# Performance work log

Hardware: AMD Instinct MI355X
Metric: run time of the kernel (lower is better)

## Reference

```python
import jax, jax.numpy as jnp
import numpy as np

D_IN, D_HIDDEN, DT_RANK, D_MEM, STEP = 256, 64, 16, 128, 16
B_, L_ = 2, 2048
S = 0.02  # weight init scale

def generate_a(d_in, d_hidden):
    i = jnp.arange(d_in, dtype=jnp.float32)[:, None]
    j = jnp.arange(d_hidden, dtype=jnp.float32)[None, :]
    off = jnp.sqrt(2.0 * i + 1.0) * jnp.sqrt(2.0 * j + 1.0)
    return jnp.where(i == j, i + 1.0, jnp.where(i > j, off, 0.0))

def setup_inputs():
    key = jax.random.key(0)
    ks = jax.random.split(key, 10)
    d_out = 3 * D_HIDDEN + 2 * D_IN + 2 * DT_RANK
    return {
        "x": jax.random.normal(ks[0], (B_, L_, D_IN), jnp.float32),
        "W_xproj": jax.random.normal(ks[1], (D_IN, d_out), jnp.float32) * S,
        "W_dt": jax.random.normal(ks[2], (DT_RANK, D_IN), jnp.float32) * S,
        "b_dt": jnp.full((D_IN,), -11.0, jnp.float32),
        "W_dtl": jax.random.normal(ks[3], (DT_RANK, D_IN), jnp.float32) * S,
        "b_dtl": jnp.full((D_IN,), -11.0, jnp.float32),
        "A": generate_a(D_IN, D_HIDDEN),
        "Dp": jnp.ones((D_IN,), jnp.float32),
        "W_Q": jax.random.normal(ks[4], (D_IN, D_MEM), jnp.float32) * S,
        "b_Q": jnp.zeros((D_MEM,), jnp.float32),
        "W_K": jax.random.normal(ks[5], (D_IN, D_MEM), jnp.float32) * S,
        "b_K": jnp.zeros((D_MEM,), jnp.float32),
        "W_V": jax.random.normal(ks[6], (D_IN, D_MEM), jnp.float32) * S,
        "b_V": jnp.zeros((D_MEM,), jnp.float32),
        "W_O": jax.random.normal(ks[7], (D_MEM, D_IN), jnp.float32) * S,
        "b_O": jnp.zeros((D_IN,), jnp.float32),
    }

def _selective_scan(u, delta, A, Bm, Cm, Dp):
    # u, delta: (b,l,d); A: (d,n); Bm, Cm: (b,l,n)
    dA = jnp.exp(jnp.einsum('bld,dn->bldn', delta, A))          # (b,l,d,n)
    dBu = delta[..., None] * Bm[:, :, None, :] * u[..., None]   # (b,l,d,n)
    def comb(e1, e2):
        a1, b1 = e1
        a2, b2 = e2
        return a2 * a1, a2 * b1 + b2
    _, xs = jax.lax.associative_scan(comb, (dA, dBu), axis=1)   # states (b,l,d,n)
    y = jnp.einsum('bldn,bln->bld', xs, Cm)
    if Dp is not None:
        y = y + u * Dp
    return y

def reference(x, W_xproj, W_dt, b_dt, W_dtl, b_dtl, A, Dp, W_Q, b_Q, W_K, b_K, W_V, b_V, W_O, b_O):
    proj = x @ W_xproj  # (b,l,3n+2d+2r)
    splits = np.cumsum([D_HIDDEN, D_HIDDEN, D_HIDDEN, D_IN, D_IN, DT_RANK]).tolist()
    Bm, Bl, Cm, E, Fg, dt, dtl = jnp.split(proj, splits, axis=-1)
    delta = jax.nn.softplus(dt @ W_dt + b_dt)       # delta_softplus=True folded in
    delta_l = jax.nn.softplus(dtl @ W_dtl + b_dtl)
    y = _selective_scan(x, delta, A, Bm, Cm, Dp)
    y_local = _selective_scan(x, delta_l, A, Bl, jnp.ones_like(Bl), None)  # C=ones, D=None
    memory = y_local[:, ::STEP, :]                  # strided checkpoints (b,m,d)
    Q = x @ W_Q + b_Q
    K = memory @ W_K + b_K
    V = memory @ W_V + b_V
    # note: original scales by sqrt(d_hidden), not sqrt(d_memory)
    w = jax.nn.softmax(jnp.einsum('blm,bkm->blk', Q, K) / jnp.sqrt(jnp.float32(D_HIDDEN)), axis=-1)
    att = jnp.einsum('blk,bkm->blm', w, V) @ W_O + b_O
    return y + att * E + x * Fg
```

## Files before the change

### kernel.cpp

```cpp
#include <hip/hip_runtime.h>
#include <math.h>

#define D_INN 256
#define D_HID 64
#define DTR 16
#define D_MEMM 128
#define BB 2
#define LL 2048
#define NROWS (BB*LL)
#define NPROJ 736
#define NTOT 864
#define SEG 16
#define SEGLEN (LL/SEG)

typedef __attribute__((ext_vector_type(8))) short short8v;
typedef __attribute__((ext_vector_type(4))) float float4v;

static __device__ __forceinline__ unsigned short f2bf(float f) {
    unsigned int u = __float_as_uint(f);
    u += 0x7fff + ((u >> 16) & 1);
    return (unsigned short)(u >> 16);
}

__global__ __launch_bounds__(256) void k_gemm(const float* __restrict__ x,
        const float* __restrict__ Wx, const float* __restrict__ Wq,
        const float* __restrict__ bq, float* __restrict__ proj) {
    __shared__ unsigned short As[64][40];
    __shared__ unsigned short Bs[64][40];
    const int t = threadIdx.x;
    const int lane = t & 63, w = t >> 6;
    const int wr = w >> 1, wc = w & 1;
    const int row0 = blockIdx.y * 64, col0 = blockIdx.x * 64;

    float4v acc[2][2];
    #pragma unroll
    for (int i = 0; i < 2; i++)
        #pragma unroll
        for (int j = 0; j < 2; j++) acc[i][j] = (float4v)0.f;

    const int ar = t >> 2, akq = (t & 3) * 8;
    const int bk = t >> 3, bcq = (t & 7) * 8;

    for (int k0 = 0; k0 < D_INN; k0 += 32) {
        float4 a0 = *(const float4*)&x[(size_t)(row0 + ar) * D_INN + k0 + akq];
        float4 a1 = *(const float4*)&x[(size_t)(row0 + ar) * D_INN + k0 + akq + 4];
        float4 b0 = {}, b1 = {};
        int col = col0 + bcq;
        if (col + 8 <= NPROJ) {
            b0 = *(const float4*)&Wx[(size_t)(k0 + bk) * NPROJ + col];
            b1 = *(const float4*)&Wx[(size_t)(k0 + bk) * NPROJ + col + 4];
        } else if (col < NTOT) {
            b0 = *(const float4*)&Wq[(size_t)(k0 + bk) * D_MEMM + (col - NPROJ)];
            b1 = *(const float4*)&Wq[(size_t)(k0 + bk) * D_MEMM + (col - NPROJ) + 4];
        }
        __syncthreads();
        {
            unsigned short av[8] = { f2bf(a0.x), f2bf(a0.y), f2bf(a0.z), f2bf(a0.w),
                                     f2bf(a1.x), f2bf(a1.y), f2bf(a1.z), f2bf(a1.w) };
            *(short8v*)&As[ar][akq] = *(short8v*)av;
            Bs[bcq + 0][bk] = f2bf(b0.x); Bs[bcq + 1][bk] = f2bf(b0.y);
            Bs[bcq + 2][bk] = f2bf(b0.z); Bs[bcq + 3][bk] = f2bf(b0.w);
            Bs[bcq + 4][bk] = f2bf(b1.x); Bs[bcq + 5][bk] = f2bf(b1.y);
            Bs[bcq + 6][bk] = f2bf(b1.z); Bs[bcq + 7][bk] = f2bf(b1.w);
        }
        __syncthreads();
        short8v af[2], bf[2];
        const int fr = lane & 15, fk = (lane >> 4) * 8;
        af[0] = *(short8v*)&As[wr * 32 + fr][fk];
        af[1] = *(short8v*)&As[wr * 32 + 16 + fr][fk];
        bf[0] = *(short8v*)&Bs[wc * 32 + fr][fk];
        bf[1] = *(short8v*)&Bs[wc * 32 + 16 + fr][fk];
        #pragma unroll
        for (int i = 0; i < 2; i++)
            #pragma unroll
            for (int j = 0; j < 2; j++)
                acc[i][j] = __builtin_amdgcn_mfma_f32_16x16x32_bf16(af[i], bf[j], acc[i][j], 0, 0, 0);
    }
    #pragma unroll
    for (int i = 0; i < 2; i++)
        #pragma unroll
        for (int j = 0; j < 2; j++)
            #pragma unroll
            for (int e = 0; e < 4; e++) {
                int rr = row0 + wr * 32 + i * 16 + (lane >> 4) * 4 + e;
                int cc = col0 + wc * 32 + j * 16 + (lane & 15);
                if (cc < NTOT) {
                    float v = acc[i][j][e];
                    if (cc >= NPROJ) v += bq[cc - NPROJ];
                    proj[(size_t)rr * NTOT + cc] = v;
                }
            }
}

__global__ __launch_bounds__(256) void k_delta(const float* __restrict__ proj,
        const float* __restrict__ Wdt, const float* __restrict__ bdt,
        const float* __restrict__ Wdtl, const float* __restrict__ bdtl,
        float* __restrict__ delta, float* __restrict__ deltal) {
    __shared__ float sdt[16][17], sdtl[16][17];
    const int t = threadIdx.x;
    const int r0 = blockIdx.x * 16;
    {
        int r = t >> 4, c = t & 15;
        sdt[r][c]  = proj[(size_t)(r0 + r) * NTOT + 704 + c];
        sdtl[r][c] = proj[(size_t)(r0 + r) * NTOT + 720 + c];
    }
    __syncthreads();
    float w1[DTR], w2[DTR];
    #pragma unroll
    for (int r = 0; r < DTR; r++) {
        w1[r] = Wdt[r * D_INN + t];
        w2[r] = Wdtl[r * D_INN + t];
    }
    const float b1 = bdt[t], b2 = bdtl[t];
    #pragma unroll
    for (int row = 0; row < 16; ++row) {
        float a1 = b1, a2 = b2;
        #pragma unroll
        for (int r = 0; r < DTR; r++) {
            a1 += sdt[row][r] * w1[r];
            a2 += sdtl[row][r] * w2[r];
        }
        delta[(size_t)(r0 + row) * D_INN + t]  = (a1 > 20.f) ? a1 : log1pf(expf(a1));
        deltal[(size_t)(r0 + row) * D_INN + t] = (a2 > 20.f) ? a2 : log1pf(expf(a2));
    }
}

__global__ __launch_bounds__(256) void k_scan1(const float* __restrict__ x,
        const float* __restrict__ proj, const float* __restrict__ A,
        const float* __restrict__ delta, const float* __restrict__ deltal,
        float* __restrict__ Qbuf, float* __restrict__ SDbuf,
        float* __restrict__ cumd, float* __restrict__ mem) {
    const int t = threadIdx.x;
    const int w = t >> 6, n = t & 63;
    const int b = blockIdx.y;
    const int scan = blockIdx.z >> 4, seg = blockIdx.z & 15;
    const int d = blockIdx.x * 4 + w;
    const size_t rowbase = (size_t)b * LL + (size_t)seg * SEGLEN;
    const float* dsel = (scan == 0 ? delta : deltal);
    const int cB = (scan == 0) ? 0 : 64;
    const float Aln = A[d * D_HID + n] * 1.44269504f;
    const int lr = n & 7;

    float s = 0.f, sd = 0.f;
    for (int c = 0; c < SEGLEN / 8; ++c) {
        const size_t l0 = rowbase + c * 8;
        float dvl = dsel[(l0 + lr) * D_INN + d];
        float pl  = dvl * x[(l0 + lr) * D_INN + d];
        float Bv[8];
        #pragma unroll
        for (int li = 0; li < 8; ++li) Bv[li] = proj[(l0 + li) * NTOT + cB + n];
        #pragma unroll
        for (int li = 0; li < 8; ++li) {
            float dv = __shfl(dvl, li);
            float p  = __shfl(pl, li);
            s = fmaf(exp2f(dv * Aln), s, p * Bv[li]);
            sd += dv;
            if (scan == 1 && li == 0 && (c & 1) == 0) {
                float v = s;
                #pragma unroll
                for (int off = 32; off >= 1; off >>= 1) v += __shfl_xor(v, off);
                if (n == 0) {
                    int k = seg * 8 + (c >> 1);
                    mem[((size_t)b * 128 + k) * D_INN + d] = v;
                    cumd[(((size_t)b * SEG + seg) * 8 + (c >> 1)) * D_INN + d] = sd;
                }
            }
        }
    }
    Qbuf[((((size_t)scan * 2 + b) * SEG + seg) * D_INN + d) * 64 + n] = s;
    if (n == 0) SDbuf[(((size_t)scan * 2 + b) * SEG + seg) * D_INN + d] = sd;
}

__global__ __launch_bounds__(256) void k_scan2(const float* __restrict__ x,
        const float* __restrict__ proj, const float* __restrict__ A,
        const float* __restrict__ Dp, const float* __restrict__ delta,
        const float* __restrict__ Qbuf, const float* __restrict__ SDbuf,
        float* __restrict__ y) {
    __shared__ float rbuf[4][8][65];
    const int t = threadIdx.x;
    const int w = t >> 6, n = t & 63;
    const int b = blockIdx.y, seg = blockIdx.z;
    const int d = blockIdx.x * 4 + w;
    const size_t rowbase = (size_t)b * LL + (size_t)seg * SEGLEN;
    const float Aln = A[d * D_HID + n] * 1.44269504f;
    const float Dpv = Dp[d];
    const int lr = n & 7;
    const int rli = n >> 3, g = n & 7;

    float s = 0.f;
    for (int k = 0; k < seg; ++k) {
        float sdk = SDbuf[(((size_t)b * SEG + k) * D_INN + d)];
        float Qk = Qbuf[(((size_t)b * SEG + k) * D_INN + d) * 64 + n];
        s = fmaf(exp2f(sdk * Aln), s, Qk);
    }

    for (int c = 0; c < SEGLEN / 8; ++c) {
        const size_t l0 = rowbase + c * 8;
        float dvl = delta[(l0 + lr) * D_INN + d];
        float uvl = x[(l0 + lr) * D_INN + d];
        float pl = dvl * uvl;
        float Bv[8], Cv[8];
        #pragma unroll
        for (int li = 0; li < 8; ++li) {
            Bv[li] = proj[(l0 + li) * NTOT + n];
            Cv[li] = proj[(l0 + li) * NTOT + 128 + n];
        }
        #pragma unroll
        for (int li = 0; li < 8; ++li) {
            float dv = __shfl(dvl, li);
            float p  = __shfl(pl, li);
            s = fmaf(exp2f(dv * Aln), s, p * Bv[li]);
            rbuf[w][li][n] = s * Cv[li];
        }
        float acc = 0.f;
        #pragma unroll
        for (int j = 0; j < 8; ++j) acc += rbuf[w][rli][g * 8 + j];
        acc += __shfl_xor(acc, 1);
        acc += __shfl_xor(acc, 2);
        acc += __shfl_xor(acc, 4);
        float uv = __shfl(uvl, rli);
        if (g == 0) {
            y[(l0 + rli) * D_INN + d] = acc + uv * Dpv;
        }
    }
}

__global__ __launch_bounds__(256) void k_sin(const float* __restrict__ A,
        const float* __restrict__ Qbuf, const float* __restrict__ SDbuf,
        float* __restrict__ Sin) {
    const int t = threadIdx.x, w = t >> 6, n = t & 63;
    const int b = blockIdx.y;
    const int d = blockIdx.x * 4 + w;
    const float Aln = A[d * D_HID + n] * 1.44269504f;
    float s = 0.f;
    #pragma unroll
    for (int seg = 0; seg < SEG; ++seg) {
        if (seg > 0) Sin[(((size_t)b * SEG + seg) * D_INN + d) * 64 + n] = s;
        float sdk = SDbuf[((size_t)(2 + b) * SEG + seg) * D_INN + d];
        float Qk = Qbuf[(((size_t)(2 + b) * SEG + seg) * D_INN + d) * 64 + n];
        s = fmaf(exp2f(sdk * Aln), s, Qk);
    }
}

__global__ __launch_bounds__(256) void k_fix(const float* __restrict__ A,
        const float* __restrict__ Sin, const float* __restrict__ cumd,
        float* __restrict__ mem) {
    const int t = threadIdx.x, w = t >> 6, n = t & 63;
    const int k = 8 + blockIdx.y;
    const int b = blockIdx.z;
    const int d = blockIdx.x * 4 + w;
    const int seg = k >> 3;
    const float Aln = A[d * D_HID + n] * 1.44269504f;
    float cum = cumd[((size_t)b * 128 + k) * D_INN + d];
    float sv = Sin[(((size_t)b * SEG + seg) * D_INN + d) * 64 + n];
    float v = exp2f(cum * Aln) * sv;
    #pragma unroll
    for (int off = 32; off >= 1; off >>= 1) v += __shfl_xor(v, off);
    if (n == 0) mem[((size_t)b * 128 + k) * D_INN + d] += v;
}

__global__ __launch_bounds__(128) void k_kvwo(const float* __restrict__ mem,
        const float* __restrict__ Wk, const float* __restrict__ bk,
        const float* __restrict__ Wv, const float* __restrict__ bv,
        const float* __restrict__ Wo,
        float* __restrict__ K, float* __restrict__ VWo) {
    __shared__ float mrow[256];
    __shared__ float vrow[128];
    const int k = blockIdx.x, b = blockIdx.y;
    const int t = threadIdx.x;
    const float* mr = mem + ((size_t)b * 128 + k) * D_INN;
    mrow[t] = mr[t];
    mrow[t + 128] = mr[t + 128];
    __syncthreads();
    float aK = bk[t], aV = bv[t];
    for (int dd = 0; dd < D_INN; dd++) {
        float m = mrow[dd];
        aK += m * Wk[dd * D_MEMM + t];
        aV += m * Wv[dd * D_MEMM + t];
    }
    K[((size_t)b * 128 + k) * D_MEMM + t] = aK;
    vrow[t] = aV;
    __syncthreads();
    float a0 = 0.f, a1 = 0.f;
    for (int m = 0; m < 128; ++m) {
        float vm = vrow[m];
        a0 += vm * Wo[(size_t)m * D_INN + t];
        a1 += vm * Wo[(size_t)m * D_INN + t + 128];
    }
    VWo[((size_t)b * 128 + k) * D_INN + t] = a0;
    VWo[((size_t)b * 128 + k) * D_INN + t + 128] = a1;
}

__global__ __launch_bounds__(256) void k_attn(const float* __restrict__ x,
        const float* __restrict__ proj, const float* __restrict__ y,
        const float* __restrict__ K, const float* __restrict__ VWo,
        const float* __restrict__ bo, float* __restrict__ out) {
    __shared__ float qs[16][132];
    __shared__ float ws[16][132];
    __shared__ float denom[16];
    const int t = threadIdx.x;
    const int b = blockIdx.y;
    const int r0 = blockIdx.x * 16;
    const size_t rowbase = (size_t)b * LL + r0;
    {
        int r = t >> 4, c8 = (t & 15) * 8;
        const float* src = &proj[(rowbase + r) * NTOT + NPROJ + c8];
        *(float4*)&qs[r][c8] = *(const float4*)src;
        *(float4*)&qs[r][c8 + 4] = *(const float4*)(src + 4);
    }
    __syncthreads();
    {
        const int k = t & 127, rg = (t >> 7) * 8;
        const float* Kr = K + ((size_t)b * 128 + k) * D_MEMM;
        float acc[8] = {};
        #pragma unroll 8
        for (int m = 0; m < 128; m += 4) {
            float4 kv = *(const float4*)&Kr[m];
            #pragma unroll
            for (int r = 0; r < 8; ++r) {
                float4 qv = *(const float4*)&qs[rg + r][m];
                acc[r] += qv.x * kv.x + qv.y * kv.y + qv.z * kv.z + qv.w * kv.w;
            }
        }
        #pragma unroll
        for (int r = 0; r < 8; ++r) ws[rg + r][k] = acc[r] * 0.125f;
    }
    __syncthreads();
    {
        const int r = t >> 4, j = t & 15;
        float4 v0 = *(float4*)&ws[r][j * 8];
        float4 v1 = *(float4*)&ws[r][j * 8 + 4];
        float mx = fmaxf(fmaxf(fmaxf(v0.x, v0.y), fmaxf(v0.z, v0.w)),
                         fmaxf(fmaxf(v1.x, v1.y), fmaxf(v1.z, v1.w)));
        #pragma unroll
        for (int o = 1; o < 16; o <<= 1) mx = fmaxf(mx, __shfl_xor(mx, o));
        v0.x = expf(v0.x - mx); v0.y = expf(v0.y - mx);
        v0.z = expf(v0.z - mx); v0.w = expf(v0.w - mx);
        v1.x = expf(v1.x - mx); v1.y = expf(v1.y - mx);
        v1.z = expf(v1.z - mx); v1.w = expf(v1.w - mx);
        float sum = v0.x + v0.y + v0.z + v0.w + v1.x + v1.y + v1.z + v1.w;
        #pragma unroll
        for (int o = 1; o < 16; o <<= 1) sum += __shfl_xor(sum, o);
        *(float4*)&ws[r][j * 8] = v0;
        *(float4*)&ws[r][j * 8 + 4] = v1;
        if (j == 0) denom[r] = sum;
    }
    __syncthreads();
    {
        const int w = t >> 6, lane = t & 63;
        const int c0 = lane * 4;
        const float* vb = VWo + (size_t)b * 128 * D_INN + c0;
        float acc[4][4] = {};
        #pragma unroll 8
        for (int k = 0; k < 128; k += 4) {
            float4 wv[4];
            #pragma unroll
            for (int r = 0; r < 4; ++r) wv[r] = *(float4*)&ws[w * 4 + r][k];
            #pragma unroll
            for (int kk = 0; kk < 4; ++kk) {
                float4 vw = *(const float4*)&vb[(size_t)(k + kk) * D_INN];
                #pragma unroll
                for (int r = 0; r < 4; ++r) {
                    float wk = (kk == 0 ? wv[r].x : kk == 1 ? wv[r].y : kk == 2 ? wv[r].z : wv[r].w);
                    acc[r][0] += wk * vw.x; acc[r][1] += wk * vw.y;
                    acc[r][2] += wk * vw.z; acc[r][3] += wk * vw.w;
                }
            }
        }
        float4 bov = *(const float4*)&bo[c0];
        #pragma unroll
        for (int r = 0; r < 4; ++r) {
            size_t rr = rowbase + w * 4 + r;
            float dn = 1.f / denom[w * 4 + r];
            float4 yv = *(const float4*)&y[rr * D_INN + c0];
            float4 xv = *(const float4*)&x[rr * D_INN + c0];
            float4 Ev = *(const float4*)&proj[rr * NTOT + 192 + c0];
            float4 Fv = *(const float4*)&proj[rr * NTOT + 448 + c0];
            float4 o;
            o.x = yv.x + (acc[r][0] * dn + bov.x) * Ev.x + xv.x * Fv.x;
            o.y = yv.y + (acc[r][1] * dn + bov.y) * Ev.y + xv.y * Fv.y;
            o.z = yv.z + (acc[r][2] * dn + bov.z) * Ev.z + xv.z * Fv.z;
            o.w = yv.w + (acc[r][3] * dn + bov.w) * Ev.w + xv.w * Fv.w;
            *(float4*)&out[rr * D_INN + c0] = o;
        }
    }
}

extern "C" void kernel_launch(void* const* d_in, const int* in_sizes, int n_in,
                              void* d_out, int out_size, void* d_ws, size_t ws_size,
                              hipStream_t stream) {
    const float* x    = (const float*)d_in[0];
    const float* Wx   = (const float*)d_in[1];
    const float* Wdt  = (const float*)d_in[2];
    const float* bdt  = (const float*)d_in[3];
    const float* Wdtl = (const float*)d_in[4];
    const float* bdtl = (const float*)d_in[5];
    const float* A    = (const float*)d_in[6];
    const float* Dp   = (const float*)d_in[7];
    const float* Wq   = (const float*)d_in[8];
    const float* bq   = (const float*)d_in[9];
    const float* Wk   = (const float*)d_in[10];
    const float* bk   = (const float*)d_in[11];
    const float* Wv   = (const float*)d_in[12];
    const float* bv   = (const float*)d_in[13];
    const float* Wo   = (const float*)d_in[14];
    const float* bo   = (const float*)d_in[15];
    float* out = (float*)d_out;
    float* ws = (float*)d_ws;

    float* proj   = ws;
    float* delta  = proj + (size_t)NROWS * NTOT;
    float* deltal = delta + (size_t)NROWS * D_INN;
    float* yb     = deltal + (size_t)NROWS * D_INN;
    float* mem    = yb + (size_t)NROWS * D_INN;
    float* Kb     = mem + (size_t)BB * 128 * D_INN;
    float* Qbuf   = Kb + (size_t)BB * 128 * D_MEMM;
    float* SDbuf  = Qbuf + (size_t)4 * SEG * D_INN * 64;
    float* cumd   = SDbuf + (size_t)4 * SEG * D_INN;
    float* Sin    = cumd + (size_t)BB * SEG * 8 * D_INN;
    float* VWo    = Sin + (size_t)BB * SEG * D_INN * 64;

    hipLaunchKernelGGL(k_gemm, dim3(14, 64), dim3(256), 0, stream, x, Wx, Wq, bq, proj);
    hipLaunchKernelGGL(k_delta, dim3(NROWS / 16), dim3(256), 0, stream,
                       proj, Wdt, bdt, Wdtl, bdtl, delta, deltal);
    hipLaunchKernelGGL(k_scan1, dim3(64, 2, 32), dim3(256), 0, stream,
                       x, proj, A, delta, deltal, Qbuf, SDbuf, cumd, mem);
    hipLaunchKernelGGL(k_scan2, dim3(64, 2, 16), dim3(256), 0, stream,
                       x, proj, A, Dp, delta, Qbuf, SDbuf, yb);
    hipLaunchKernelGGL(k_sin, dim3(64, 2), dim3(256), 0, stream,
                       A, Qbuf, SDbuf, Sin);
    hipLaunchKernelGGL(k_fix, dim3(64, 120, 2), dim3(256), 0, stream,
                       A, Sin, cumd, mem);
    hipLaunchKernelGGL(k_kvwo, dim3(128, 2), dim3(128), 0, stream,
                       mem, Wk, bk, Wv, bv, Wo, Kb, VWo);
    hipLaunchKernelGGL(k_attn, dim3(128, 2), dim3(256), 0, stream,
                       x, proj, yb, Kb, VWo, bo, out);
}
```

Baseline: 228.2 us.

## Store delta and x transposed for contiguous scan loads, use readlane broadcasts

Adds a transpose kernel that writes x as (b,d,l), and makes the delta kernel write delta and delta_l in the same transposed layout with float4 stores. The two scan kernels then load 8 consecutive timesteps for one channel from contiguous memory instead of from addresses a full row apart. Lane broadcasts in the scan loops switch from __shfl to readlane intrinsics, which avoid LDS-based permutes. In exchange there is an extra kernel launch and an extra pass over x, and the delta writes in k_delta become strided per thread.

```diff
diff --git a/kernel.cpp b/kernel.cpp
--- a/kernel.cpp
+++ b/kernel.cpp
@@ -22,6 +22,10 @@
     return (unsigned short)(u >> 16);
 }
 
+static __device__ __forceinline__ float rdlane(float v, int l) {
+    return __uint_as_float(__builtin_amdgcn_readlane(__float_as_uint(v), l));
+}
+
 __global__ __launch_bounds__(256) void k_gemm(const float* __restrict__ x,
         const float* __restrict__ Wx, const float* __restrict__ Wq,
         const float* __restrict__ bq, float* __restrict__ proj) {
@@ -92,13 +96,29 @@
             }
 }
 
+__global__ __launch_bounds__(256) void k_xt(const float* __restrict__ x,
+        float* __restrict__ xT) {
+    __shared__ float tile[64][65];
+    const int t = threadIdx.x;
+    const int lt = blockIdx.x * 64, dt = blockIdx.y * 64, b = blockIdx.z;
+    const int c = t & 63, rg = (t >> 6) * 16;
+    #pragma unroll
+    for (int j = 0; j < 16; ++j)
+        tile[rg + j][c] = x[((size_t)b * LL + lt + rg + j) * D_INN + dt + c];
+    __syncthreads();
+    #pragma unroll
+    for (int j = 0; j < 16; ++j)
+        xT[((size_t)b * D_INN + dt + rg + j) * LL + lt + c] = tile[c][rg + j];
+}
+
 __global__ __launch_bounds__(256) void k_delta(const float* __restrict__ proj,
         const float* __restrict__ Wdt, const float* __restrict__ bdt,
         const float* __restrict__ Wdtl, const float* __restrict__ bdtl,
-        float* __restrict__ delta, float* __restrict__ deltal) {
+        float* __restrict__ deltaT, float* __restrict__ deltalT) {
     __shared__ float sdt[16][17], sdtl[16][17];
     const int t = threadIdx.x;
     const int r0 = blockIdx.x * 16;
+    const int b = r0 >> 11, l0 = r0 & (LL - 1);
     {
         int r = t >> 4, c = t & 15;
         sdt[r][c]  = proj[(size_t)(r0 + r) * NTOT + 704 + c];
@@ -112,6 +132,7 @@
         w2[r] = Wdtl[r * D_INN + t];
     }
     const float b1 = bdt[t], b2 = bdtl[t];
+    float o1[16], o2[16];
     #pragma unroll
     for (int row = 0; row < 16; ++row) {
         float a1 = b1, a2 = b2;
@@ -120,14 +141,21 @@
             a1 += sdt[row][r] * w1[r];
             a2 += sdtl[row][r] * w2[r];
         }
-        delta[(size_t)(r0 + row) * D_INN + t]  = (a1 > 20.f) ? a1 : log1pf(expf(a1));
-        deltal[(size_t)(r0 + row) * D_INN + t] = (a2 > 20.f) ? a2 : log1pf(expf(a2));
-    }
-}
-
-__global__ __launch_bounds__(256) void k_scan1(const float* __restrict__ x,
+        o1[row] = (a1 > 20.f) ? a1 : log1pf(expf(a1));
+        o2[row] = (a2 > 20.f) ? a2 : log1pf(expf(a2));
+    }
+    float* p1 = &deltaT[((size_t)b * D_INN + t) * LL + l0];
+    float* p2 = &deltalT[((size_t)b * D_INN + t) * LL + l0];
+    #pragma unroll
+    for (int j = 0; j < 16; j += 4) {
+        *(float4*)&p1[j] = make_float4(o1[j], o1[j+1], o1[j+2], o1[j+3]);
+        *(float4*)&p2[j] = make_float4(o2[j], o2[j+1], o2[j+2], o2[j+3]);
+    }
+}
+
+__global__ __launch_bounds__(256) void k_scan1(const float* __restrict__ xT,
         const float* __restrict__ proj, const float* __restrict__ A,
-        const float* __restrict__ delta, const float* __restrict__ deltal,
+        const float* __restrict__ deltaT, const float* __restrict__ deltalT,
         float* __restrict__ Qbuf, float* __restrict__ SDbuf,
         float* __restrict__ cumd, float* __restrict__ mem) {
     const int t = threadIdx.x;
@@ -136,7 +164,8 @@
     const int scan = blockIdx.z >> 4, seg = blockIdx.z & 15;
     const int d = blockIdx.x * 4 + w;
     const size_t rowbase = (size_t)b * LL + (size_t)seg * SEGLEN;
-    const float* dsel = (scan == 0 ? delta : deltal);
+    const float* dT = (scan == 0 ? deltaT : deltalT) + ((size_t)b * D_INN + d) * LL + seg * SEGLEN;
+    const float* uT = xT + ((size_t)b * D_INN + d) * LL + seg * SEGLEN;
     const int cB = (scan == 0) ? 0 : 64;
     const float Aln = A[d * D_HID + n] * 1.44269504f;
     const int lr = n & 7;
@@ -144,15 +173,15 @@
     float s = 0.f, sd = 0.f;
     for (int c = 0; c < SEGLEN / 8; ++c) {
         const size_t l0 = rowbase + c * 8;
-        float dvl = dsel[(l0 + lr) * D_INN + d];
-        float pl  = dvl * x[(l0 + lr) * D_INN + d];
+        float dvl = dT[c * 8 + lr];
+        float pl  = dvl * uT[c * 8 + lr];
         float Bv[8];
         #pragma unroll
         for (int li = 0; li < 8; ++li) Bv[li] = proj[(l0 + li) * NTOT + cB + n];
         #pragma unroll
         for (int li = 0; li < 8; ++li) {
-            float dv = __shfl(dvl, li);
-            float p  = __shfl(pl, li);
+            float dv = rdlane(dvl, li);
+            float p  = rdlane(pl, li);
             s = fmaf(exp2f(dv * Aln), s, p * Bv[li]);
             sd += dv;
             if (scan == 1 && li == 0 && (c & 1) == 0) {
@@ -171,9 +200,9 @@
     if (n == 0) SDbuf[(((size_t)scan * 2 + b) * SEG + seg) * D_INN + d] = sd;
 }
 
-__global__ __launch_bounds__(256) void k_scan2(const float* __restrict__ x,
+__global__ __launch_bounds__(256) void k_scan2(const float* __restrict__ xT,
         const float* __restrict__ proj, const float* __restrict__ A,
-        const float* __restrict__ Dp, const float* __restrict__ delta,
+        const float* __restrict__ Dp, const float* __restrict__ deltaT,
         const float* __restrict__ Qbuf, const float* __restrict__ SDbuf,
         float* __restrict__ y) {
     __shared__ float rbuf[4][8][65];
@@ -182,6 +211,8 @@
     const int b = blockIdx.y, seg = blockIdx.z;
     const int d = blockIdx.x * 4 + w;
     const size_t rowbase = (size_t)b * LL + (size_t)seg * SEGLEN;
+    const float* dT = deltaT + ((size_t)b * D_INN + d) * LL + seg * SEGLEN;
+    const float* uT = xT + ((size_t)b * D_INN + d) * LL + seg * SEGLEN;
     const float Aln = A[d * D_HID + n] * 1.44269504f;
     const float Dpv = Dp[d];
     const int lr = n & 7;
@@ -196,8 +227,8 @@
 
     for (int c = 0; c < SEGLEN / 8; ++c) {
         const size_t l0 = rowbase + c * 8;
-        float dvl = delta[(l0 + lr) * D_INN + d];
-        float uvl = x[(l0 + lr) * D_INN + d];
+        float dvl = dT[c * 8 + lr];
+        float uvl = uT[c * 8 + lr];
         float pl = dvl * uvl;
         float Bv[8], Cv[8];
         #pragma unroll
@@ -207,8 +238,8 @@
         }
         #pragma unroll
         for (int li = 0; li < 8; ++li) {
-            float dv = __shfl(dvl, li);
-            float p  = __shfl(pl, li);
+            float dv = rdlane(dvl, li);
+            float p  = rdlane(pl, li);
             s = fmaf(exp2f(dv * Aln), s, p * Bv[li]);
             rbuf[w][li][n] = s * Cv[li];
         }
@@ -408,25 +439,27 @@
     float* out = (float*)d_out;
     float* ws = (float*)d_ws;
 
-    float* proj   = ws;
-    float* delta  = proj + (size_t)NROWS * NTOT;
-    float* deltal = delta + (size_t)NROWS * D_INN;
-    float* yb     = deltal + (size_t)NROWS * D_INN;
-    float* mem    = yb + (size_t)NROWS * D_INN;
-    float* Kb     = mem + (size_t)BB * 128 * D_INN;
-    float* Qbuf   = Kb + (size_t)BB * 128 * D_MEMM;
-    float* SDbuf  = Qbuf + (size_t)4 * SEG * D_INN * 64;
-    float* cumd   = SDbuf + (size_t)4 * SEG * D_INN;
-    float* Sin    = cumd + (size_t)BB * SEG * 8 * D_INN;
-    float* VWo    = Sin + (size_t)BB * SEG * D_INN * 64;
+    float* proj    = ws;
+    float* deltaT  = proj + (size_t)NROWS * NTOT;
+    float* deltalT = deltaT + (size_t)NROWS * D_INN;
+    float* yb      = deltalT + (size_t)NROWS * D_INN;
+    float* mem     = yb + (size_t)NROWS * D_INN;
+    float* Kb      = mem + (size_t)BB * 128 * D_INN;
+    float* Qbuf    = Kb + (size_t)BB * 128 * D_MEMM;
+    float* SDbuf   = Qbuf + (size_t)4 * SEG * D_INN * 64;
+    float* cumd    = SDbuf + (size_t)4 * SEG * D_INN;
+    float* Sin     = cumd + (size_t)BB * SEG * 8 * D_INN;
+    float* VWo     = Sin + (size_t)BB * SEG * D_INN * 64;
+    float* xT      = VWo + (size_t)BB * 128 * D_INN;
 
     hipLaunchKernelGGL(k_gemm, dim3(14, 64), dim3(256), 0, stream, x, Wx, Wq, bq, proj);
+    hipLaunchKernelGGL(k_xt, dim3(32, 4, 2), dim3(256), 0, stream, x, xT);
     hipLaunchKernelGGL(k_delta, dim3(NROWS / 16), dim3(256), 0, stream,
-                       proj, Wdt, bdt, Wdtl, bdtl, delta, deltal);
+                       proj, Wdt, bdt, Wdtl, bdtl, deltaT, deltalT);
     hipLaunchKernelGGL(k_scan1, dim3(64, 2, 32), dim3(256), 0, stream,
-                       x, proj, A, delta, deltal, Qbuf, SDbuf, cumd, mem);
+                       xT, proj, A, deltaT, deltalT, Qbuf, SDbuf, cumd, mem);
     hipLaunchKernelGGL(k_scan2, dim3(64, 2, 16), dim3(256), 0, stream,
-                       x, proj, A, Dp, delta, Qbuf, SDbuf, yb);
+                       xT, proj, A, Dp, deltaT, Qbuf, SDbuf, yb);
     hipLaunchKernelGGL(k_sin, dim3(64, 2), dim3(256), 0, stream,
                        A, Qbuf, SDbuf, Sin);
     hipLaunchKernelGGL(k_fix, dim3(64, 120, 2), dim3(256), 0, stream,
```

Measured after the change: 222.7 us. -2.4%, faster.
